# Optimization experiments

Hardware: AMD Instinct MI355X
Metric: run time of the kernel (lower is better)

## Reference

```python
import jax, jax.numpy as jnp
import numpy as np

GRID_N = 3   # number of grid intervals (pykan 'grid')
K = 3        # spline order (pykan 'k')
IN_F = 512
OUT_F = 512
BATCH = 8
SEQ = 2048


def _extended_grid(d, dtype):
    # base grid: num+1 points over [-1, 1]; extend by K steps of h on each side (pykan extend_grid)
    pts = jnp.linspace(-1.0, 1.0, GRID_N + 1).astype(dtype)
    h = jnp.asarray(2.0 / GRID_N, dtype)
    left = pts[0] + h * jnp.arange(-K, 0, dtype=dtype)
    right = pts[-1] + h * jnp.arange(1, K + 1, dtype=dtype)
    ext = jnp.concatenate([left, pts, right])           # (GRID_N + 1 + 2K,)
    return jnp.broadcast_to(ext, (d, ext.shape[0]))     # per-input-feature grid (shared values)


def _bspline_basis(x, grid):
    # Cox-de Boor recursion, vectorized over tokens and input features.
    # x: (N, D), grid: (D, M) -> returns (N, D, M-1-K) = (N, D, GRID_N+K)
    x = x[:, :, None]                     # (N, D, 1)
    g = grid[None, :, :]                  # (1, D, M)
    B = ((x >= g[..., :-1]) & (x < g[..., 1:])).astype(x.dtype)
    for p in range(1, K + 1):
        left = (x - g[..., :-(p + 1)]) / (g[..., p:-1] - g[..., :-(p + 1)])
        right = (g[..., p + 1:] - x) / (g[..., p + 1:] - g[..., 1:-p])
        B = left * B[..., :-1] + right * B[..., 1:]
    return B


def setup_inputs() -> dict:
    key = jax.random.key(0)
    k1, k2, k3 = jax.random.split(key, 3)
    x = jax.random.normal(k1, (BATCH, SEQ, IN_F), dtype=jnp.float32)
    coef = jax.random.normal(k2, (OUT_F, IN_F, GRID_N + K), dtype=jnp.float32) * 0.1
    scale_base = (1.0 / np.sqrt(IN_F)) + (jax.random.uniform(k3, (OUT_F, IN_F), dtype=jnp.float32) * 2.0 - 1.0) * 0.1
    scale_sp = jnp.ones((OUT_F, IN_F), dtype=jnp.float32)
    bias = jnp.zeros((OUT_F,), dtype=jnp.float32)
    return {"x": x, "coef": coef, "scale_base": scale_base, "scale_sp": scale_sp, "bias": bias}


def reference(x, coef, scale_base, scale_sp, bias):
    B_, S, D = x.shape
    xf = x.reshape(-1, D)                               # (N, D) tokens
    grid = _extended_grid(D, xf.dtype)
    basis = _bspline_basis(xf, grid)                    # (N, D, GRID_N+K)
    base = jax.nn.silu(xf)                              # base activation per input feature
    # per-edge: scale_base*silu(x_i) + scale_sp*spline(x_i); sum over input features, add bias
    spline_w = scale_sp[..., None] * coef               # (O, D, GRID_N+K)
    y = (jnp.einsum('ni,oi->no', base, scale_base)
         + jnp.einsum('nib,oib->no', basis, spline_w)
         + bias[None, :])
    return y.reshape(B_, S, -1)
```

## Files before the change

kernel.cpp:

```cpp
#include <hip/hip_runtime.h>


typedef short        bf16x8 __attribute__((ext_vector_type(8)));
typedef float        f32x4  __attribute__((ext_vector_type(4)));
typedef unsigned int u32x4  __attribute__((ext_vector_type(4)));

#define NROWS 16384
#define DIN   512
#define DOUT  512
#define BM    128
#define BN    256
#define NKT   64

__device__ __forceinline__ unsigned short f2bf(float f) {
    unsigned int u = __float_as_uint(f);
    u += 0x7fffu + ((u >> 16) & 1u);
    return (unsigned short)(u >> 16);
}

__device__ __forceinline__ void kan_act_store(float xv, char* p16) {
    float S  = __builtin_fmaf(xv, 1.5f, 4.5f);
    float jf = floorf(S);
    float t  = S - jf;
    int   j  = (int)jf;
    float t2 = t * t;
    float t3 = t2 * t;
    float omt  = 1.0f - t;
    float omt2 = omt * omt;
    float n0 = omt2 * omt * (1.0f / 6.0f);
    float n1 = __builtin_fmaf(t3, 0.5f, -t2) + (2.0f / 3.0f);
    float u  = (t + t2) - t3;
    float n2 = __builtin_fmaf(u, 0.5f, 1.0f / 6.0f);
    float n3 = t3 * (1.0f / 6.0f);
    float e  = __expf(-xv);
    float si = xv * __builtin_amdgcn_rcpf(1.0f + e);

    unsigned w01, w23, wsil;
    asm("v_cvt_pk_bf16_f32 %0, %1, %2" : "=v"(w01)  : "v"(n0), "v"(n1));
    asm("v_cvt_pk_bf16_f32 %0, %1, %2" : "=v"(w23)  : "v"(n2), "v"(n3));
    asm("v_cvt_pk_bf16_f32 %0, %1, %2" : "=v"(wsil) : "v"(si), "v"(0.0f));

    u32x4 init = {wsil, 0u, 0u, 0u};
    *(u32x4*)p16 = init;

    unsigned short v0 = (unsigned short)w01, v1 = (unsigned short)(w01 >> 16);
    unsigned short v2 = (unsigned short)w23, v3 = (unsigned short)(w23 >> 16);
    int b0 = j - 3;
    int s0 = ((unsigned)(b0    ) <= 5u) ? (b0 + 1) : 7;
    int s1 = ((unsigned)(b0 + 1) <= 5u) ? (b0 + 2) : 7;
    int s2 = ((unsigned)(b0 + 2) <= 5u) ? (b0 + 3) : 7;
    int s3 = ((unsigned)(b0 + 3) <= 5u) ? (b0 + 4) : 7;
    *(unsigned short*)(p16 + 2 * s0) = v0;
    *(unsigned short*)(p16 + 2 * s1) = v1;
    *(unsigned short*)(p16 + 2 * s2) = v2;
    *(unsigned short*)(p16 + 2 * s3) = v3;
}

__global__ __launch_bounds__(256) void kan_prep(
    const float* __restrict__ coef, const float* __restrict__ scale_base,
    const float* __restrict__ scale_sp, unsigned short* __restrict__ wt)
{
    int t = blockIdx.x * 256 + threadIdx.x;
    int o = t >> 9;
    int i = t & 511;
    float sb = scale_base[t];
    float sp = scale_sp[t];
    const float* cp = coef + (size_t)t * 6;
    bf16x8 w;
    w[0] = (short)f2bf(sb);
#pragma unroll
    for (int b = 0; b < 6; ++b) w[1 + b] = (short)f2bf(sp * cp[b]);
    w[7] = 0;
    int nt = o >> 8, ol = o & 255;
    int kt = i >> 3, s = i & 7, ks = s >> 2, fg = s & 3;
    size_t off = (size_t)nt * 2097152
               + (size_t)((kt * 2 + ks) * 256 + ol) * 64 + fg * 16;
    *(bf16x8*)((char*)wt + off) = w;
}

__global__ __launch_bounds__(512, 2) void kan_gemm(
    const float* __restrict__ x, const unsigned short* __restrict__ wt,
    const float* __restrict__ bias, float* __restrict__ y)
{
    __shared__ char As[2][BM * 128];

    const int tid  = threadIdx.x;
    const int lane = tid & 63;
    const int wid  = tid >> 6;
    const int wm   = wid >> 2;
    const int wn   = wid & 3;

    int bid = blockIdx.x;
    int wg  = (bid & 7) * 32 + (bid >> 3);
    int mt  = wg & 127;
    int nt  = wg >> 7;

    const int row0 = mt * BM;
    const int col0 = nt * BN;

    const int ar = tid >> 2;
    const int ap = tid & 3;
    const float* xp = x + (size_t)(row0 + ar) * DIN + ap * 2;
    const int as_sw = (ar & 7) << 4;
    const int c0 = (ap * 2) << 4;

    const int fr = lane & 15;
    const int fg = lane >> 4;

    const char* wb = (const char*)wt + (size_t)nt * 2097152;
    int colpart[4];
#pragma unroll
    for (int n2 = 0; n2 < 4; ++n2)
        colpart[n2] = (wn * 64 + n2 * 16 + fr) * 64 + fg * 16;

#define LOADB_H(B, ktv, ks_)                                                  \
    {                                                                         \
        const char* wkt_ = wb + (size_t)((ktv) * 2 + (ks_)) * 16384;          \
        _Pragma("unroll")                                                     \
        for (int n2_ = 0; n2_ < 4; ++n2_)                                     \
            B[(ks_) * 4 + n2_] = *(const bf16x8*)(wkt_ + colpart[n2_]);       \
    }

    f32x4 acc[4][4];
#pragma unroll
    for (int m2 = 0; m2 < 4; ++m2)
#pragma unroll
        for (int n2 = 0; n2 < 4; ++n2) {
            f32x4 z = {0.f, 0.f, 0.f, 0.f};
            acc[m2][n2] = z;
        }

    bf16x8 Ba[8], Bb[8];

    LOADB_H(Ba, 0, 0);
    LOADB_H(Ba, 0, 1);
    {
        float2 xa = *(const float2*)(xp);
        char* rowp = &As[0][ar * 128];
        kan_act_store(xa.x, rowp + (c0 ^ as_sw));
        kan_act_store(xa.y, rowp + ((c0 + 16) ^ as_sw));
    }
    float2 xb = *(const float2*)(xp + 8);
    asm volatile("s_waitcnt lgkmcnt(0)" ::: "memory");
    __builtin_amdgcn_s_barrier();

#define STEP(ktv, Bcur, Bnext)                                                \
    {                                                                         \
        const int cur_ = (ktv) & 1, nxt_ = cur_ ^ 1;                          \
        const bool hn_ = (ktv) + 1 < NKT;                                     \
        char* rowp_ = &As[nxt_][ar * 128];                                    \
        bf16x8 af_[2][4];                                                     \
        _Pragma("unroll")                                                     \
        for (int ks_ = 0; ks_ < 2; ++ks_) {                                   \
            _Pragma("unroll")                                                 \
            for (int m2_ = 0; m2_ < 4; ++m2_) {                               \
                int rr_ = wm * 64 + m2_ * 16 + fr;                            \
                af_[ks_][m2_] = *(const bf16x8*)(&As[cur_][0] + rr_ * 128     \
                    + ((ks_ * 64 + fg * 16) ^ ((rr_ & 7) << 4)));             \
            }                                                                 \
        }                                                                     \
        if (hn_) LOADB_H(Bnext, (ktv) + 1, 0);                                \
        if (hn_) kan_act_store(xb.x, rowp_ + (c0 ^ as_sw));                   \
        _Pragma("unroll")                                                     \
        for (int m2_ = 0; m2_ < 4; ++m2_)                                     \
            _Pragma("unroll")                                                 \
            for (int n2_ = 0; n2_ < 4; ++n2_)                                 \
                acc[m2_][n2_] = __builtin_amdgcn_mfma_f32_16x16x32_bf16(      \
                    af_[0][m2_], Bcur[n2_], acc[m2_][n2_], 0, 0, 0);          \
        if (hn_) LOADB_H(Bnext, (ktv) + 1, 1);                                \
        if (hn_) {                                                            \
            kan_act_store(xb.y, rowp_ + ((c0 + 16) ^ as_sw));                 \
            if ((ktv) + 2 < NKT)                                              \
                xb = *(const float2*)(xp + ((ktv) + 2) * 8);                  \
        }                                                                     \
        _Pragma("unroll")                                                     \
        for (int m2_ = 0; m2_ < 4; ++m2_)                                     \
            _Pragma("unroll")                                                 \
            for (int n2_ = 0; n2_ < 4; ++n2_)                                 \
                acc[m2_][n2_] = __builtin_amdgcn_mfma_f32_16x16x32_bf16(      \
                    af_[1][m2_], Bcur[4 + n2_], acc[m2_][n2_], 0, 0, 0);      \
        asm volatile("s_waitcnt lgkmcnt(0)" ::: "memory");                    \
        __builtin_amdgcn_s_barrier();                                         \
    }

    for (int kt = 0; kt < NKT; kt += 2) {
        STEP(kt, Ba, Bb);
        STEP(kt + 1, Bb, Ba);
    }

    const int orow0 = row0 + wm * 64 + fg * 4;
    const int ocol0 = col0 + wn * 64 + fr;
#pragma unroll
    for (int n2 = 0; n2 < 4; ++n2) {
        float bv = bias[ocol0 + n2 * 16];
#pragma unroll
        for (int m2 = 0; m2 < 4; ++m2) {
#pragma unroll
            for (int r = 0; r < 4; ++r) {
                y[(size_t)(orow0 + m2 * 16 + r) * DOUT + (ocol0 + n2 * 16)]
                    = acc[m2][n2][r] + bv;
            }
        }
    }
#undef STEP
#undef LOADB_H
}

extern "C" void kernel_launch(void* const* d_in, const int* in_sizes, int n_in,
                              void* d_out, int out_size, void* d_ws, size_t ws_size,
                              hipStream_t stream)
{
    const float* x          = (const float*)d_in[0];
    const float* coef       = (const float*)d_in[1];
    const float* scale_base = (const float*)d_in[2];
    const float* scale_sp   = (const float*)d_in[3];
    const float* bias       = (const float*)d_in[4];
    unsigned short* wt = (unsigned short*)d_ws;
    float* y = (float*)d_out;

    kan_prep<<<1024, 256, 0, stream>>>(coef, scale_base, scale_sp, wt);
    kan_gemm<<<256, 512, 0, stream>>>(x, wt, bias, y);
}
```

Before: 96.21 us.

## Halve GEMM row tile, drop B register prefetch, raise occupancy to four blocks

```diff
diff --git a/kernel.cpp b/kernel.cpp
--- a/kernel.cpp
+++ b/kernel.cpp
@@ -8,7 +8,7 @@
 #define NROWS 16384
 #define DIN   512
 #define DOUT  512
-#define BM    128
+#define BM    64
 #define BN    256
 #define NKT   64
 
@@ -78,7 +78,7 @@
     *(bf16x8*)((char*)wt + off) = w;
 }
 
-__global__ __launch_bounds__(512, 2) void kan_gemm(
+__global__ __launch_bounds__(512, 4) void kan_gemm(
     const float* __restrict__ x, const unsigned short* __restrict__ wt,
     const float* __restrict__ bias, float* __restrict__ y)
 {
@@ -91,18 +91,20 @@
     const int wn   = wid & 3;
 
     int bid = blockIdx.x;
-    int wg  = (bid & 7) * 32 + (bid >> 3);
-    int mt  = wg & 127;
-    int nt  = wg >> 7;
+    int wg  = (bid & 7) * 64 + (bid >> 3);
+    int mt  = wg & 255;
+    int nt  = wg >> 8;
 
     const int row0 = mt * BM;
     const int col0 = nt * BN;
 
-    const int ar = tid >> 2;
-    const int ap = tid & 3;
-    const float* xp = x + (size_t)(row0 + ar) * DIN + ap * 2;
+    const int ar = tid >> 3;
+    const int ap = tid & 7;
+    const float* xp = x + (size_t)(row0 + ar) * DIN + ap;
     const int as_sw = (ar & 7) << 4;
-    const int c0 = (ap * 2) << 4;
+    const int c0 = ap << 4;
+    char* const arow0p = &As[0][ar * 128];
+    char* const arow1p = &As[1][ar * 128];
 
     const int fr = lane & 15;
     const int fg = lane >> 4;
@@ -118,83 +120,74 @@
         const char* wkt_ = wb + (size_t)((ktv) * 2 + (ks_)) * 16384;          \
         _Pragma("unroll")                                                     \
         for (int n2_ = 0; n2_ < 4; ++n2_)                                     \
-            B[(ks_) * 4 + n2_] = *(const bf16x8*)(wkt_ + colpart[n2_]);       \
-    }
-
-    f32x4 acc[4][4];
-#pragma unroll
-    for (int m2 = 0; m2 < 4; ++m2)
+            B[n2_] = *(const bf16x8*)(wkt_ + colpart[n2_]);                   \
+    }
+
+    f32x4 acc[2][4];
+#pragma unroll
+    for (int m2 = 0; m2 < 2; ++m2)
 #pragma unroll
         for (int n2 = 0; n2 < 4; ++n2) {
             f32x4 z = {0.f, 0.f, 0.f, 0.f};
             acc[m2][n2] = z;
         }
 
-    bf16x8 Ba[8], Bb[8];
-
-    LOADB_H(Ba, 0, 0);
-    LOADB_H(Ba, 0, 1);
-    {
-        float2 xa = *(const float2*)(xp);
-        char* rowp = &As[0][ar * 128];
-        kan_act_store(xa.x, rowp + (c0 ^ as_sw));
-        kan_act_store(xa.y, rowp + ((c0 + 16) ^ as_sw));
-    }
-    float2 xb = *(const float2*)(xp + 8);
+    kan_act_store(xp[0], arow0p + (c0 ^ as_sw));
+    float xb = xp[8];
     asm volatile("s_waitcnt lgkmcnt(0)" ::: "memory");
     __builtin_amdgcn_s_barrier();
 
-#define STEP(ktv, Bcur, Bnext)                                                \
+#define STEP(ktv)                                                             \
     {                                                                         \
-        const int cur_ = (ktv) & 1, nxt_ = cur_ ^ 1;                          \
-        const bool hn_ = (ktv) + 1 < NKT;                                     \
-        char* rowp_ = &As[nxt_][ar * 128];                                    \
-        bf16x8 af_[2][4];                                                     \
+        const int cur_ = (ktv) & 1;                                           \
+        bf16x8 af_[2][2];                                                     \
         _Pragma("unroll")                                                     \
         for (int ks_ = 0; ks_ < 2; ++ks_) {                                   \
             _Pragma("unroll")                                                 \
-            for (int m2_ = 0; m2_ < 4; ++m2_) {                               \
-                int rr_ = wm * 64 + m2_ * 16 + fr;                            \
+            for (int m2_ = 0; m2_ < 2; ++m2_) {                               \
+                int rr_ = wm * 32 + m2_ * 16 + fr;                            \
                 af_[ks_][m2_] = *(const bf16x8*)(&As[cur_][0] + rr_ * 128     \
                     + ((ks_ * 64 + fg * 16) ^ ((rr_ & 7) << 4)));             \
             }                                                                 \
         }                                                                     \
-        if (hn_) LOADB_H(Bnext, (ktv) + 1, 0);                                \
-        if (hn_) kan_act_store(xb.x, rowp_ + (c0 ^ as_sw));                   \
-        _Pragma("unroll")                                                     \
-        for (int m2_ = 0; m2_ < 4; ++m2_)                                     \
+        bf16x8 B0_[4], B1_[4];                                                \
+        LOADB_H(B0_, ktv, 0);                                                 \
+        LOADB_H(B1_, ktv, 1);                                                 \
+        if ((ktv) + 1 < NKT) {                                                \
+            char* rowp_ = (((ktv) + 1) & 1) ? arow1p : arow0p;                \
+            kan_act_store(xb, rowp_ + (c0 ^ as_sw));                          \
+            if ((ktv) + 2 < NKT) xb = xp[((ktv) + 2) * 8];                    \
+        }                                                                     \
+        __builtin_amdgcn_s_setprio(1);                                        \
+        _Pragma("unroll")                                                     \
+        for (int m2_ = 0; m2_ < 2; ++m2_)                                     \
             _Pragma("unroll")                                                 \
             for (int n2_ = 0; n2_ < 4; ++n2_)                                 \
                 acc[m2_][n2_] = __builtin_amdgcn_mfma_f32_16x16x32_bf16(      \
-                    af_[0][m2_], Bcur[n2_], acc[m2_][n2_], 0, 0, 0);          \
-        if (hn_) LOADB_H(Bnext, (ktv) + 1, 1);                                \
-        if (hn_) {                                                            \
-            kan_act_store(xb.y, rowp_ + ((c0 + 16) ^ as_sw));                 \
-            if ((ktv) + 2 < NKT)                                              \
-                xb = *(const float2*)(xp + ((ktv) + 2) * 8);                  \
-        }                                                                     \
-        _Pragma("unroll")                                                     \
-        for (int m2_ = 0; m2_ < 4; ++m2_)                                     \
+                    af_[0][m2_], B0_[n2_], acc[m2_][n2_], 0, 0, 0);           \
+        _Pragma("unroll")                                                     \
+        for (int m2_ = 0; m2_ < 2; ++m2_)                                     \
             _Pragma("unroll")                                                 \
             for (int n2_ = 0; n2_ < 4; ++n2_)                                 \
                 acc[m2_][n2_] = __builtin_amdgcn_mfma_f32_16x16x32_bf16(      \
-                    af_[1][m2_], Bcur[4 + n2_], acc[m2_][n2_], 0, 0, 0);      \
+                    af_[1][m2_], B1_[n2_], acc[m2_][n2_], 0, 0, 0);           \
+        __builtin_amdgcn_s_setprio(0);                                        \
         asm volatile("s_waitcnt lgkmcnt(0)" ::: "memory");                    \
         __builtin_amdgcn_s_barrier();                                         \
     }
 
     for (int kt = 0; kt < NKT; kt += 2) {
-        STEP(kt, Ba, Bb);
-        STEP(kt + 1, Bb, Ba);
-    }
-
-    const int orow0 = row0 + wm * 64 + fg * 4;
+        STEP(kt);
+        STEP(kt + 1);
+    }
+
+    const int orow0 = row0 + wm * 32 + fg * 4;
     const int ocol0 = col0 + wn * 64 + fr;
 #pragma unroll
     for (int n2 = 0; n2 < 4; ++n2) {
         float bv = bias[ocol0 + n2 * 16];
 #pragma unroll
-        for (int m2 = 0; m2 < 4; ++m2) {
+        for (int m2 = 0; m2 < 2; ++m2) {
 #pragma unroll
             for (int r = 0; r < 4; ++r) {
                 y[(size_t)(orow0 + m2 * 16 + r) * DOUT + (ocol0 + n2 * 16)]
@@ -219,5 +212,5 @@
     float* y = (float*)d_out;
 
     kan_prep<<<1024, 256, 0, stream>>>(coef, scale_base, scale_sp, wt);
-    kan_gemm<<<256, 512, 0, stream>>>(x, wt, bias, y);
-}
+    kan_gemm<<<512, 512, 0, stream>>>(x, wt, bias, y);
+}
```

After: 144.3 us. +50.0%, slower.
